# Kernel tuning notes

Hardware: AMD Instinct MI355X
Metric: run time of the kernel (lower is better)

Reference implementation:

```python
import jax, jax.numpy as jnp
import numpy as np

IN, H1, H2, H3, H4, OUT = 512, 2048, 2048, 1024, 512, 1


def setup_inputs() -> dict:
    key = jax.random.key(0)
    ks = jax.random.split(key, 12)
    def lin(k, fan_in, fan_out):
        # torch Linear default init: U(-1/sqrt(fan_in), 1/sqrt(fan_in))
        bound = 1.0 / np.sqrt(fan_in)
        k1, k2 = jax.random.split(k)
        W = jax.random.uniform(k1, (fan_out, fan_in), jnp.float32, -bound, bound)
        b = jax.random.uniform(k2, (fan_out,), jnp.float32, -bound, bound)
        return W, b
    x = jax.random.normal(ks[0], (16384, IN), jnp.float32)
    cross_w = jnp.ones((IN,), jnp.float32)   # init.constant_(1.0)
    cross_b = jnp.zeros((IN,), jnp.float32)  # init.constant_(0.0)
    W1, b1 = lin(ks[1], IN, H1)
    W2, b2 = lin(ks[2], H1, H2)
    W3, b3 = lin(ks[3], H2, H3)
    W4, b4 = lin(ks[4], H3, H4)
    Wo, bo = lin(ks[5], H4, OUT)
    return {"x": x, "cross_w": cross_w, "cross_b": cross_b,
            "W1": W1, "b1": b1, "W2": W2, "b2": b2,
            "W3": W3, "b3": b3, "W4": W4, "b4": b4,
            "Wo": Wo, "bo": bo}


def reference(x, cross_w, cross_b, W1, b1, W2, b2, W3, b3, W4, b4, Wo, bo):
    # Cross layer: bmm(x0[...,None], x[...,None,:]) . w == x0 * (x . w)
    # (mathematically identical, avoids the O(f^2) outer product)
    xw = x @ cross_w                         # [B]
    h = x * xw[:, None] + cross_b + x        # [B, IN]
    h = jax.nn.relu(h @ W1.T + b1)           # [B, H1]
    h = jax.nn.relu(h @ W2.T + b2)           # [B, H2]
    h = jax.nn.relu(h @ W3.T + b3)           # [B, H3]
    h = jax.nn.relu(h @ W4.T + b4)           # [B, H4]
    return h @ Wo.T + bo                     # [B, OUT]
```

## Files before the change

### kernel.cpp

```cpp
#include <hip/hip_runtime.h>


#define BM 128
#define BN 256
#define BK 64

typedef __bf16 bf16x8 __attribute__((ext_vector_type(8)));
typedef float  f32x4  __attribute__((ext_vector_type(4)));
typedef unsigned short u16x4 __attribute__((ext_vector_type(4)));

__device__ __forceinline__ unsigned short f2bf(float f) {
    unsigned int u = __builtin_bit_cast(unsigned int, f);
    u += 0x7fffu + ((u >> 16) & 1u);
    return (unsigned short)(u >> 16);
}
__device__ __forceinline__ float bf2f(unsigned short h) {
    unsigned int u = ((unsigned int)h) << 16;
    return __builtin_bit_cast(float, u);
}

__device__ __forceinline__ void async16(const void* g, void* l) {
    __builtin_amdgcn_global_load_lds(
        (const __attribute__((address_space(1))) unsigned int*)g,
        (__attribute__((address_space(3))) unsigned int*)l,
        16, 0, 0);
}

__global__ __launch_bounds__(256, 2)
void gemm_bt_bias_relu(const unsigned short* __restrict__ A,
                       const unsigned short* __restrict__ B,
                       const float* __restrict__ bias,
                       unsigned short* __restrict__ C,
                       int M, int N, int K)
{
    __shared__ __align__(16) unsigned short As[BM * BK];
    __shared__ __align__(16) unsigned short Bs[BN * BK];

    const int tid  = threadIdx.x;
    const int lane = tid & 63;
    const int wave = tid >> 6;
    const int quad = lane >> 4;
    const int l16  = lane & 15;

    const int bm = blockIdx.x * BM;
    const int bn = blockIdx.y * BN;
    const int wm = (wave & 1) * 64;
    const int wn = (wave >> 1) * 128;

    const int lrow = tid >> 3;
    const int gcol = ((tid & 7) ^ (lrow & 7)) * 8;

    const unsigned short* gaBase = A + (size_t)(bm + lrow) * K + gcol;
    const unsigned short* gbBase = B + (size_t)(bn + lrow) * K + gcol;

    unsigned short* lA = As + tid * 8;
    unsigned short* lB = Bs + tid * 8;

    const int xa = l16 & 7;
    const unsigned short* As_w = As + (wm + l16) * BK;
    const unsigned short* Bs_w = Bs + (wn + l16) * BK;
    const int c0 = (quad ^ xa) * 8;
    const int c1 = ((quad ^ 4) ^ xa) * 8;

    f32x4 acc[4][8] = {};

    for (int k0 = 0; k0 < K; k0 += BK) {
#pragma unroll
        for (int i = 0; i < 4; ++i)
            async16(gaBase + (size_t)(i * 32) * K + k0, lA + i * 2048);
#pragma unroll
        for (int i = 0; i < 8; ++i)
            async16(gbBase + (size_t)(i * 32) * K + k0, lB + i * 2048);
        __syncthreads();

#pragma unroll
        for (int kk = 0; kk < 2; ++kk) {
            const int cs = kk ? c1 : c0;
            bf16x8 af[4], bfr[8];
#pragma unroll
            for (int i = 0; i < 4; ++i) af[i]  = *(const bf16x8*)(As_w + i * 16 * BK + cs);
#pragma unroll
            for (int j = 0; j < 8; ++j) bfr[j] = *(const bf16x8*)(Bs_w + j * 16 * BK + cs);
#pragma unroll
            for (int i = 0; i < 4; ++i)
#pragma unroll
                for (int j = 0; j < 8; ++j)
                    acc[i][j] = __builtin_amdgcn_mfma_f32_16x16x32_bf16(
                        af[i], bfr[j], acc[i][j], 0, 0, 0);
        }
        __syncthreads();
    }

    float bv[8];
#pragma unroll
    for (int j = 0; j < 8; ++j) bv[j] = bias[bn + wn + j * 16 + l16];

#pragma unroll
    for (int i = 0; i < 4; ++i) {
        const int row0 = bm + wm + i * 16 + quad * 4;
#pragma unroll
        for (int j = 0; j < 8; ++j) {
            const int col = bn + wn + j * 16 + l16;
#pragma unroll
            for (int r = 0; r < 4; ++r) {
                float v = acc[i][j][r] + bv[j];
                v = fmaxf(v, 0.0f);
                C[(size_t)(row0 + r) * N + col] = f2bf(v);
            }
        }
    }
}

__global__ __launch_bounds__(256)
void cross_kernel(const float* __restrict__ x, const float* __restrict__ cw,
                  const float* __restrict__ cb, unsigned short* __restrict__ h0)
{
    const int row  = blockIdx.x * 4 + (threadIdx.x >> 6);
    const int lane = threadIdx.x & 63;
    const float* xr = x + (size_t)row * 512;
    float xv[8];
    float s = 0.f;
#pragma unroll
    for (int i = 0; i < 8; ++i) {
        const int c = lane + i * 64;
        xv[i] = xr[c];
        s += xv[i] * cw[c];
    }
#pragma unroll
    for (int off = 32; off > 0; off >>= 1) s += __shfl_down(s, off, 64);
    s = __shfl(s, 0, 64);
    unsigned short* hr = h0 + (size_t)row * 512;
#pragma unroll
    for (int i = 0; i < 8; ++i) {
        const int c = lane + i * 64;
        hr[c] = f2bf(xv[i] * s + cb[c] + xv[i]);
    }
}

__global__ __launch_bounds__(256)
void final_dot(const unsigned short* __restrict__ h4, const float* __restrict__ Wo,
               const float* __restrict__ bo, float* __restrict__ out)
{
    const int row  = blockIdx.x * 4 + (threadIdx.x >> 6);
    const int lane = threadIdx.x & 63;
    const unsigned short* hr = h4 + (size_t)row * 512;
    float s = 0.f;
#pragma unroll
    for (int i = 0; i < 8; ++i) {
        const int c = lane + i * 64;
        s += bf2f(hr[c]) * Wo[c];
    }
#pragma unroll
    for (int off = 32; off > 0; off >>= 1) s += __shfl_down(s, off, 64);
    if (lane == 0) out[row] = s + bo[0];
}

__global__ __launch_bounds__(256)
void convert_weights(const float* __restrict__ s1, const float* __restrict__ s2,
                     const float* __restrict__ s3, const float* __restrict__ s4,
                     unsigned short* __restrict__ d1, unsigned short* __restrict__ d2,
                     unsigned short* __restrict__ d3, unsigned short* __restrict__ d4)
{
    long t = (long)blockIdx.x * 256 + threadIdx.x;
    const float* s; unsigned short* d; long off;
    if (t < 262144L)       { s = s1; d = d1; off = t; }
    else if (t < 1310720L) { s = s2; d = d2; off = t - 262144L; }
    else if (t < 1835008L) { s = s3; d = d3; off = t - 1310720L; }
    else                   { s = s4; d = d4; off = t - 1835008L; }
    f32x4 f = *(const f32x4*)(s + off * 4);
    u16x4 o;
#pragma unroll
    for (int i = 0; i < 4; ++i) o[i] = f2bf(f[i]);
    *(u16x4*)(d + off * 4) = o;
}

extern "C" void kernel_launch(void* const* d_in, const int* in_sizes, int n_in,
                              void* d_out, int out_size, void* d_ws, size_t ws_size,
                              hipStream_t stream)
{
    const float* x  = (const float*)d_in[0];
    const float* cw = (const float*)d_in[1];
    const float* cb = (const float*)d_in[2];
    const float* W1 = (const float*)d_in[3];  const float* b1 = (const float*)d_in[4];
    const float* W2 = (const float*)d_in[5];  const float* b2 = (const float*)d_in[6];
    const float* W3 = (const float*)d_in[7];  const float* b3 = (const float*)d_in[8];
    const float* W4 = (const float*)d_in[9];  const float* b4 = (const float*)d_in[10];
    const float* Wo = (const float*)d_in[11]; const float* bo = (const float*)d_in[12];
    float* out = (float*)d_out;

    char* p = (char*)d_ws;
    unsigned short* wb1 = (unsigned short*)p; p += (size_t)2048 * 512  * 2;
    unsigned short* wb2 = (unsigned short*)p; p += (size_t)2048 * 2048 * 2;
    unsigned short* wb3 = (unsigned short*)p; p += (size_t)1024 * 2048 * 2;
    unsigned short* wb4 = (unsigned short*)p; p += (size_t)512  * 1024 * 2;
    unsigned short* actA = (unsigned short*)p; p += (size_t)16384 * 2048 * 2;
    unsigned short* actB = (unsigned short*)p;

    convert_weights<<<7680, 256, 0, stream>>>(W1, W2, W3, W4, wb1, wb2, wb3, wb4);
    cross_kernel<<<4096, 256, 0, stream>>>(x, cw, cb, actA);

    gemm_bt_bias_relu<<<dim3(128, 8), 256, 0, stream>>>(actA, wb1, b1, actB, 16384, 2048, 512);
    gemm_bt_bias_relu<<<dim3(128, 8), 256, 0, stream>>>(actB, wb2, b2, actA, 16384, 2048, 2048);
    gemm_bt_bias_relu<<<dim3(128, 4), 256, 0, stream>>>(actA, wb3, b3, actB, 16384, 1024, 2048);
    gemm_bt_bias_relu<<<dim3(128, 2), 256, 0, stream>>>(actB, wb4, b4, actA, 16384, 512, 1024);
    final_dot<<<4096, 256, 0, stream>>>(actA, Wo, bo, out);
}
```

Baseline: 355.6 us.

## Double-buffer B tiles, prefetch A via registers, fuse prep kernels, retile last GEMM

The GEMM mainloop double-buffers the B tile in LDS with async global-to-LDS loads and prefetches the next A tile into registers while computing the current tile. The goal is to overlap memory latency with MFMA work. The weight-conversion and cross-layer kernels are merged into a single launch, and the last GEMM uses a narrower N tile to launch more blocks. The cost is more LDS and registers per block, which may reduce occupancy, plus an extra barrier per iteration.

```diff
diff --git a/kernel.cpp b/kernel.cpp
--- a/kernel.cpp
+++ b/kernel.cpp
@@ -1,8 +1,6 @@
 #include <hip/hip_runtime.h>
 
 
-#define BM 128
-#define BN 256
 #define BK 64
 
 typedef __bf16 bf16x8 __attribute__((ext_vector_type(8)));
@@ -26,6 +24,7 @@
         16, 0, 0);
 }
 
+template<int BN>
 __global__ __launch_bounds__(256, 2)
 void gemm_bt_bias_relu(const unsigned short* __restrict__ A,
                        const unsigned short* __restrict__ B,
@@ -33,8 +32,9 @@
                        unsigned short* __restrict__ C,
                        int M, int N, int K)
 {
-    __shared__ __align__(16) unsigned short As[BM * BK];
-    __shared__ __align__(16) unsigned short Bs[BN * BK];
+    constexpr int JT = BN / 32;
+    __shared__ __align__(16) unsigned short As[128 * BK];
+    __shared__ __align__(16) unsigned short Bs[2 * BN * BK];
 
     const int tid  = threadIdx.x;
     const int lane = tid & 63;
@@ -42,10 +42,10 @@
     const int quad = lane >> 4;
     const int l16  = lane & 15;
 
-    const int bm = blockIdx.x * BM;
+    const int bm = blockIdx.x * 128;
     const int bn = blockIdx.y * BN;
     const int wm = (wave & 1) * 64;
-    const int wn = (wave >> 1) * 128;
+    const int wn = (wave >> 1) * (BN / 2);
 
     const int lrow = tid >> 3;
     const int gcol = ((tid & 7) ^ (lrow & 7)) * 8;
@@ -54,52 +54,78 @@
     const unsigned short* gbBase = B + (size_t)(bn + lrow) * K + gcol;
 
     unsigned short* lA = As + tid * 8;
-    unsigned short* lB = Bs + tid * 8;
 
     const int xa = l16 & 7;
     const unsigned short* As_w = As + (wm + l16) * BK;
-    const unsigned short* Bs_w = Bs + (wn + l16) * BK;
     const int c0 = (quad ^ xa) * 8;
     const int c1 = ((quad ^ 4) ^ xa) * 8;
 
-    f32x4 acc[4][8] = {};
-
-    for (int k0 = 0; k0 < K; k0 += BK) {
-#pragma unroll
-        for (int i = 0; i < 4; ++i)
-            async16(gaBase + (size_t)(i * 32) * K + k0, lA + i * 2048);
-#pragma unroll
-        for (int i = 0; i < 8; ++i)
-            async16(gbBase + (size_t)(i * 32) * K + k0, lB + i * 2048);
-        __syncthreads();
-
+    f32x4 acc[4][JT] = {};
+    bf16x8 areg[4];
+
+    auto compute = [&](const unsigned short* Bsb) {
+        const unsigned short* Bw = Bsb + (wn + l16) * BK;
 #pragma unroll
         for (int kk = 0; kk < 2; ++kk) {
             const int cs = kk ? c1 : c0;
-            bf16x8 af[4], bfr[8];
-#pragma unroll
-            for (int i = 0; i < 4; ++i) af[i]  = *(const bf16x8*)(As_w + i * 16 * BK + cs);
-#pragma unroll
-            for (int j = 0; j < 8; ++j) bfr[j] = *(const bf16x8*)(Bs_w + j * 16 * BK + cs);
+            bf16x8 af[4], bfr[JT];
+#pragma unroll
+            for (int i = 0; i < 4; ++i)  af[i]  = *(const bf16x8*)(As_w + i * 16 * BK + cs);
+#pragma unroll
+            for (int j = 0; j < JT; ++j) bfr[j] = *(const bf16x8*)(Bw + j * 16 * BK + cs);
 #pragma unroll
             for (int i = 0; i < 4; ++i)
 #pragma unroll
-                for (int j = 0; j < 8; ++j)
+                for (int j = 0; j < JT; ++j)
                     acc[i][j] = __builtin_amdgcn_mfma_f32_16x16x32_bf16(
                         af[i], bfr[j], acc[i][j], 0, 0, 0);
         }
+    };
+
+    const int nk = K / BK;
+
+#pragma unroll
+    for (int i = 0; i < 4; ++i)
+        areg[i] = *(const bf16x8*)(gaBase + (size_t)(i * 32) * K);
+    {
+        unsigned short* lB0 = Bs + tid * 8;
+#pragma unroll
+        for (int i = 0; i < JT; ++i)
+            async16(gbBase + (size_t)(i * 32) * K, lB0 + i * 2048);
+    }
+#pragma unroll
+    for (int i = 0; i < 4; ++i)
+        *(bf16x8*)(lA + i * 2048) = areg[i];
+    __syncthreads();
+
+    for (int k = 0; k < nk - 1; ++k) {
+        const size_t k0n = (size_t)(k + 1) * BK;
+#pragma unroll
+        for (int i = 0; i < 4; ++i)
+            areg[i] = *(const bf16x8*)(gaBase + (size_t)(i * 32) * K + k0n);
+        unsigned short* lBn = Bs + ((k + 1) & 1) * (BN * BK) + tid * 8;
+#pragma unroll
+        for (int i = 0; i < JT; ++i)
+            async16(gbBase + (size_t)(i * 32) * K + k0n, lBn + i * 2048);
+
+        compute(Bs + (k & 1) * (BN * BK));
         __syncthreads();
-    }
-
-    float bv[8];
-#pragma unroll
-    for (int j = 0; j < 8; ++j) bv[j] = bias[bn + wn + j * 16 + l16];
+#pragma unroll
+        for (int i = 0; i < 4; ++i)
+            *(bf16x8*)(lA + i * 2048) = areg[i];
+        __syncthreads();
+    }
+    compute(Bs + ((nk - 1) & 1) * (BN * BK));
+
+    float bv[JT];
+#pragma unroll
+    for (int j = 0; j < JT; ++j) bv[j] = bias[bn + wn + j * 16 + l16];
 
 #pragma unroll
     for (int i = 0; i < 4; ++i) {
         const int row0 = bm + wm + i * 16 + quad * 4;
 #pragma unroll
-        for (int j = 0; j < 8; ++j) {
+        for (int j = 0; j < JT; ++j) {
             const int col = bn + wn + j * 16 + l16;
 #pragma unroll
             for (int r = 0; r < 4; ++r) {
@@ -112,28 +138,47 @@
 }
 
 __global__ __launch_bounds__(256)
-void cross_kernel(const float* __restrict__ x, const float* __restrict__ cw,
-                  const float* __restrict__ cb, unsigned short* __restrict__ h0)
-{
-    const int row  = blockIdx.x * 4 + (threadIdx.x >> 6);
-    const int lane = threadIdx.x & 63;
-    const float* xr = x + (size_t)row * 512;
-    float xv[8];
-    float s = 0.f;
-#pragma unroll
-    for (int i = 0; i < 8; ++i) {
-        const int c = lane + i * 64;
-        xv[i] = xr[c];
-        s += xv[i] * cw[c];
-    }
-#pragma unroll
-    for (int off = 32; off > 0; off >>= 1) s += __shfl_down(s, off, 64);
-    s = __shfl(s, 0, 64);
-    unsigned short* hr = h0 + (size_t)row * 512;
-#pragma unroll
-    for (int i = 0; i < 8; ++i) {
-        const int c = lane + i * 64;
-        hr[c] = f2bf(xv[i] * s + cb[c] + xv[i]);
+void prep_kernel(const float* __restrict__ x, const float* __restrict__ cw,
+                 const float* __restrict__ cb, unsigned short* __restrict__ h0,
+                 const float* __restrict__ s1, const float* __restrict__ s2,
+                 const float* __restrict__ s3, const float* __restrict__ s4,
+                 unsigned short* __restrict__ d1, unsigned short* __restrict__ d2,
+                 unsigned short* __restrict__ d3, unsigned short* __restrict__ d4)
+{
+    const int b = blockIdx.x;
+    if (b < 7680) {
+        long t = (long)b * 256 + threadIdx.x;
+        const float* s; unsigned short* d; long off;
+        if (t < 262144L)       { s = s1; d = d1; off = t; }
+        else if (t < 1310720L) { s = s2; d = d2; off = t - 262144L; }
+        else if (t < 1835008L) { s = s3; d = d3; off = t - 1310720L; }
+        else                   { s = s4; d = d4; off = t - 1835008L; }
+        f32x4 f = *(const f32x4*)(s + off * 4);
+        u16x4 o;
+#pragma unroll
+        for (int i = 0; i < 4; ++i) o[i] = f2bf(f[i]);
+        *(u16x4*)(d + off * 4) = o;
+    } else {
+        const int row  = (b - 7680) * 4 + (threadIdx.x >> 6);
+        const int lane = threadIdx.x & 63;
+        const float* xr = x + (size_t)row * 512;
+        float xv[8];
+        float s = 0.f;
+#pragma unroll
+        for (int i = 0; i < 8; ++i) {
+            const int c = lane + i * 64;
+            xv[i] = xr[c];
+            s += xv[i] * cw[c];
+        }
+#pragma unroll
+        for (int off = 32; off > 0; off >>= 1) s += __shfl_down(s, off, 64);
+        s = __shfl(s, 0, 64);
+        unsigned short* hr = h0 + (size_t)row * 512;
+#pragma unroll
+        for (int i = 0; i < 8; ++i) {
+            const int c = lane + i * 64;
+            hr[c] = f2bf(xv[i] * s + cb[c] + xv[i]);
+        }
     }
 }
 
@@ -153,25 +198,6 @@
 #pragma unroll
     for (int off = 32; off > 0; off >>= 1) s += __shfl_down(s, off, 64);
     if (lane == 0) out[row] = s + bo[0];
-}
-
-__global__ __launch_bounds__(256)
-void convert_weights(const float* __restrict__ s1, const float* __restrict__ s2,
-                     const float* __restrict__ s3, const float* __restrict__ s4,
-                     unsigned short* __restrict__ d1, unsigned short* __restrict__ d2,
-                     unsigned short* __restrict__ d3, unsigned short* __restrict__ d4)
-{
-    long t = (long)blockIdx.x * 256 + threadIdx.x;
-    const float* s; unsigned short* d; long off;
-    if (t < 262144L)       { s = s1; d = d1; off = t; }
-    else if (t < 1310720L) { s = s2; d = d2; off = t - 262144L; }
-    else if (t < 1835008L) { s = s3; d = d3; off = t - 1310720L; }
-    else                   { s = s4; d = d4; off = t - 1835008L; }
-    f32x4 f = *(const f32x4*)(s + off * 4);
-    u16x4 o;
-#pragma unroll
-    for (int i = 0; i < 4; ++i) o[i] = f2bf(f[i]);
-    *(u16x4*)(d + off * 4) = o;
 }
 
 extern "C" void kernel_launch(void* const* d_in, const int* in_sizes, int n_in,
@@ -196,12 +222,12 @@
     unsigned short* actA = (unsigned short*)p; p += (size_t)16384 * 2048 * 2;
     unsigned short* actB = (unsigned short*)p;
 
-    convert_weights<<<7680, 256, 0, stream>>>(W1, W2, W3, W4, wb1, wb2, wb3, wb4);
-    cross_kernel<<<4096, 256, 0, stream>>>(x, cw, cb, actA);
-
-    gemm_bt_bias_relu<<<dim3(128, 8), 256, 0, stream>>>(actA, wb1, b1, actB, 16384, 2048, 512);
-    gemm_bt_bias_relu<<<dim3(128, 8), 256, 0, stream>>>(actB, wb2, b2, actA, 16384, 2048, 2048);
-    gemm_bt_bias_relu<<<dim3(128, 4), 256, 0, stream>>>(actA, wb3, b3, actB, 16384, 1024, 2048);
-    gemm_bt_bias_relu<<<dim3(128, 2), 256, 0, stream>>>(actB, wb4, b4, actA, 16384, 512, 1024);
+    prep_kernel<<<11776, 256, 0, stream>>>(x, cw, cb, actA,
+                                           W1, W2, W3, W4, wb1, wb2, wb3, wb4);
+
+    gemm_bt_bias_relu<256><<<dim3(128, 8), 256, 0, stream>>>(actA, wb1, b1, actB, 16384, 2048, 512);
+    gemm_bt_bias_relu<256><<<dim3(128, 8), 256, 0, stream>>>(actB, wb2, b2, actA, 16384, 2048, 2048);
+    gemm_bt_bias_relu<256><<<dim3(128, 4), 256, 0, stream>>>(actA, wb3, b3, actB, 16384, 1024, 2048);
+    gemm_bt_bias_relu<128><<<dim3(128, 4), 256, 0, stream>>>(actB, wb4, b4, actA, 16384, 512, 1024);
     final_dot<<<4096, 256, 0, stream>>>(actA, Wo, bo, out);
 }
```

New measurement: 375.5 us. +5.6%, slower.
